# Performance work log

Measured on AMD Instinct MI355X. Metric: run time of the kernel, lower is better.

Reference implementation:

```python
import jax, jax.numpy as jnp
import numpy as np

B, N, D, DH = 2, 256, 256, 256


def setup_inputs() -> dict:
    key = jax.random.key(0)
    ks = jax.random.split(key, 8)
    s = 1.0 / np.sqrt(D)
    return {
        "x": jax.random.normal(ks[0], (B, N, D), dtype=jnp.float32),
        "e": jax.random.normal(ks[1], (B, N, N, D), dtype=jnp.float32),
        "Wq": jax.random.normal(ks[2], (D, DH), dtype=jnp.float32) * s,
        "bq": jnp.zeros((DH,), dtype=jnp.float32),
        "Wk": jax.random.normal(ks[3], (D, DH), dtype=jnp.float32) * s,
        "bk": jnp.zeros((DH,), dtype=jnp.float32),
        "Wv": jax.random.normal(ks[4], (D, DH), dtype=jnp.float32) * s,
        "bv": jnp.zeros((DH,), dtype=jnp.float32),
    }


def reference(x, e, Wq, bq, Wk, bk, Wv, bv):
    # Q_edge: [B, N, N, DH]; indexed Q[b, j, i, :]
    Q = jnp.einsum("bjid,dh->bjih", e, Wq) + bq
    K = x @ Wk + bk  # [B, N, DH]
    V = x @ Wv + bv  # [B, N, DH]
    scale = 1.0 / jnp.sqrt(jnp.asarray(Q.shape[-1], Q.dtype))
    # K_i[b,j,i] = K[b,i];  K_j[b,j,i] = K[b,j]  (torch expand semantics)
    att_i = jnp.exp(jnp.einsum("bjih,bih->bji", Q, K) * scale)
    att_j = jnp.exp(jnp.einsum("bjih,bjh->bji", Q, K) * scale)
    att_sum = att_i + att_j
    ai = att_i / att_sum  # dropout with p=0.0 is identity
    aj = att_j / att_sum
    # e_out[b,j,i] = ai*V[b,i] + aj*V[b,j]
    e_out = ai[..., None] * V[:, None, :, :] + aj[..., None] * V[:, :, None, :]
    return (x, e_out)
```

## Files before the change

### kernel.cpp

```cpp
#include <hip/hip_runtime.h>
#include <hip/hip_bf16.h>

typedef __bf16 bf16_t;
typedef bf16_t bf16x8 __attribute__((ext_vector_type(8)));
typedef float  f32x4  __attribute__((ext_vector_type(4)));

constexpr int Bc  = 2;
constexpr int Nc  = 256;
constexpr int Dc  = 256;
constexpr int DHc = 256;
constexpr int BM  = 64;
constexpr int NIB = Nc / BM;

__global__ void prep_kv(const float* __restrict__ x,
                        const float* __restrict__ Wk, const float* __restrict__ bk,
                        const float* __restrict__ Wv, const float* __restrict__ bv,
                        float* __restrict__ Kd, float* __restrict__ Vd) {
    constexpr int RPB = 4;
    __shared__ float xs[RPB][Dc];
    int r0 = blockIdx.x * RPB;
    int h  = threadIdx.x;
    for (int rr = 0; rr < RPB; ++rr)
        xs[rr][h] = x[(size_t)(r0 + rr) * Dc + h];
    __syncthreads();
    float bkv = bk[h], bvv = bv[h];
    float ka[RPB], va[RPB];
    #pragma unroll
    for (int rr = 0; rr < RPB; ++rr) { ka[rr] = bkv; va[rr] = bvv; }
    for (int d = 0; d < Dc; ++d) {
        float wk = Wk[(size_t)d * DHc + h];
        float wv = Wv[(size_t)d * DHc + h];
        #pragma unroll
        for (int rr = 0; rr < RPB; ++rr) {
            ka[rr] += xs[rr][d] * wk;
            va[rr] += xs[rr][d] * wv;
        }
    }
    #pragma unroll
    for (int rr = 0; rr < RPB; ++rr) {
        Kd[(size_t)(r0 + rr) * DHc + h] = ka[rr];
        Vd[(size_t)(r0 + rr) * DHc + h] = va[rr];
    }
}

__global__ void prep_wqt(const float* __restrict__ Wq, bf16_t* __restrict__ WqT) {
    int n = blockIdx.x;
    int d = threadIdx.x;
    WqT[(size_t)n * Dc + d] = (bf16_t)Wq[(size_t)d * DHc + n];
}

struct SMu {
    union {
        struct {
            bf16_t A[BM][Dc + 8];
            bf16_t Bt[DHc][40];
        } g;
        float Q[BM][DHc + 4];
    };
};

__global__ __launch_bounds__(256, 2)
void edge_attn(const float* __restrict__ e,
               const float* __restrict__ bq,
               const bf16_t* __restrict__ WqT,
               const float* __restrict__ Kd,
               const float* __restrict__ Vd,
               float* __restrict__ eout) {
    __shared__ SMu sm;
    __shared__ float s_kj[DHc], s_vj[DHc], s_bq[DHc];
    __shared__ float s_ri[BM][4], s_rj[BM][4];
    __shared__ float s_ai[BM], s_aj[BM];

    const int bid = blockIdx.x;
    const int b   = bid / (Nc * NIB);
    const int rem = bid % (Nc * NIB);
    const int j   = rem / NIB;
    const int i0  = (rem % NIB) * BM;
    const int tid = threadIdx.x;
    const int l   = tid & 63;
    const int w   = tid >> 6;
    const int lr  = l & 15;
    const int lk  = (l >> 4) * 8;

    {
        size_t off = ((size_t)b * Nc + j) * DHc + tid;
        s_kj[tid] = Kd[off];
        s_vj[tid] = Vd[off];
        s_bq[tid] = bq[tid];
    }

    const float4* e4 = reinterpret_cast<const float4*>(
        e + (((size_t)b * Nc + j) * Nc + i0) * Dc);
    #pragma unroll
    for (int q = 0; q < 16; ++q) {
        int f = tid + q * 256;
        float4 v = e4[f];
        int r = f >> 6;
        int c = (f & 63) * 4;
        union { bf16_t h[4]; uint2 u; } p;
        p.h[0] = (bf16_t)v.x; p.h[1] = (bf16_t)v.y;
        p.h[2] = (bf16_t)v.z; p.h[3] = (bf16_t)v.w;
        *reinterpret_cast<uint2*>(&sm.g.A[r][c]) = p.u;
    }

    f32x4 acc[4][4] = {};
    for (int ks = 0; ks < Dc / 32; ++ks) {
        const int k0 = ks * 32;
        __syncthreads();
        {
            const uint4* src = reinterpret_cast<const uint4*>(
                WqT + (size_t)tid * Dc + k0);
            uint4* dst = reinterpret_cast<uint4*>(&sm.g.Bt[tid][0]);
            dst[0] = src[0]; dst[1] = src[1]; dst[2] = src[2]; dst[3] = src[3];
        }
        __syncthreads();
        bf16x8 a[4], bb[4];
        #pragma unroll
        for (int m = 0; m < 4; ++m)
            a[m] = *reinterpret_cast<const bf16x8*>(&sm.g.A[m * 16 + lr][k0 + lk]);
        #pragma unroll
        for (int n = 0; n < 4; ++n)
            bb[n] = *reinterpret_cast<const bf16x8*>(&sm.g.Bt[w * 64 + n * 16 + lr][lk]);
        #pragma unroll
        for (int m = 0; m < 4; ++m)
            #pragma unroll
            for (int n = 0; n < 4; ++n)
                acc[m][n] = __builtin_amdgcn_mfma_f32_16x16x32_bf16(
                    a[m], bb[n], acc[m][n], 0, 0, 0);
    }
    __syncthreads();

    #pragma unroll
    for (int m = 0; m < 4; ++m) {
        int row0 = m * 16 + (l >> 4) * 4;
        #pragma unroll
        for (int n = 0; n < 4; ++n) {
            int col = w * 64 + n * 16 + lr;
            float bqv = s_bq[col];
            #pragma unroll
            for (int qq = 0; qq < 4; ++qq)
                sm.Q[row0 + qq][col] = acc[m][n][qq] + bqv;
        }
    }
    __syncthreads();

    {
        const int r = l;
        const int p = w;
        const float4* Krow = reinterpret_cast<const float4*>(
            Kd + (((size_t)b * Nc) + i0 + r) * DHc + p * 64);
        const float4* Qrow = reinterpret_cast<const float4*>(&sm.Q[r][p * 64]);
        const float4* Kj4  = reinterpret_cast<const float4*>(&s_kj[p * 64]);
        float si = 0.f, sj = 0.f;
        #pragma unroll
        for (int c4 = 0; c4 < 16; ++c4) {
            float4 qv = Qrow[c4];
            float4 ki = Krow[c4];
            float4 kj = Kj4[c4];
            si += qv.x * ki.x + qv.y * ki.y + qv.z * ki.z + qv.w * ki.w;
            sj += qv.x * kj.x + qv.y * kj.y + qv.z * kj.z + qv.w * kj.w;
        }
        s_ri[r][p] = si;
        s_rj[r][p] = sj;
    }
    __syncthreads();
    if (tid < BM) {
        float si = s_ri[tid][0] + s_ri[tid][1] + s_ri[tid][2] + s_ri[tid][3];
        float sj = s_rj[tid][0] + s_rj[tid][1] + s_rj[tid][2] + s_rj[tid][3];
        constexpr float scale = 0.0625f;
        float ai = 1.f / (1.f + __expf((sj - si) * scale));
        s_ai[tid] = ai;
        s_aj[tid] = 1.f - ai;
    }
    __syncthreads();

    {
        const int cg = (tid & 63) * 4;
        const int ro = tid >> 6;
        const float* Vb = Vd + ((size_t)b * Nc + i0) * DHc;
        float* ob = eout + (((size_t)b * Nc + j) * Nc + i0) * DHc;
        float4 vj = *reinterpret_cast<const float4*>(&s_vj[cg]);
        #pragma unroll
        for (int q = 0; q < 16; ++q) {
            int r = q * 4 + ro;
            float aiv = s_ai[r], ajv = s_aj[r];
            float4 vi = *reinterpret_cast<const float4*>(Vb + (size_t)r * DHc + cg);
            float4 o;
            o.x = aiv * vi.x + ajv * vj.x;
            o.y = aiv * vi.y + ajv * vj.y;
            o.z = aiv * vi.z + ajv * vj.z;
            o.w = aiv * vi.w + ajv * vj.w;
            *reinterpret_cast<float4*>(ob + (size_t)r * DHc + cg) = o;
        }
    }
}

extern "C" void kernel_launch(void* const* d_in, const int* in_sizes, int n_in,
                              void* d_out, int out_size, void* d_ws, size_t ws_size,
                              hipStream_t stream) {
    const float* x  = (const float*)d_in[0];
    const float* e  = (const float*)d_in[1];
    const float* Wq = (const float*)d_in[2];
    const float* bq = (const float*)d_in[3];
    const float* Wk = (const float*)d_in[4];
    const float* bk = (const float*)d_in[5];
    const float* Wv = (const float*)d_in[6];
    const float* bv = (const float*)d_in[7];
    float* out = (float*)d_out;

    float*  Kd  = (float*)d_ws;
    float*  Vd  = Kd + (size_t)Bc * Nc * DHc;
    bf16_t* WqT = (bf16_t*)(Vd + (size_t)Bc * Nc * DHc);

    hipMemcpyAsync(out, x, (size_t)Bc * Nc * Dc * sizeof(float),
                   hipMemcpyDeviceToDevice, stream);

    prep_kv<<<Bc * Nc / 4, 256, 0, stream>>>(x, Wk, bk, Wv, bv, Kd, Vd);
    prep_wqt<<<DHc, Dc, 0, stream>>>(Wq, WqT);
    edge_attn<<<Bc * Nc * NIB, 256, 0, stream>>>(
        e, bq, WqT, Kd, Vd, out + (size_t)Bc * Nc * Dc);
}
```

Measured before the change: 327.5 us.

## Fold Wq into K to replace edge GEMM with per-edge dot products

The score Q·K is rewritten as e·(Wq K) plus bq·K, so a prep kernel computes G = Wq·K (pre-scaled) and a bias term per node. The edge kernel then streams e once and takes two dot products per row with wavefront shuffle reductions, dropping the bf16 MFMA GEMM, the shared-memory staging and the Wq transpose kernel. The main kernel becomes a pure memory stream over e and the output, and it keeps full fp32 precision instead of bf16 for e.

```diff
diff --git a/kernel.cpp b/kernel.cpp
--- a/kernel.cpp
+++ b/kernel.cpp
@@ -1,9 +1,5 @@
 #include <hip/hip_runtime.h>
 #include <hip/hip_bf16.h>
-
-typedef __bf16 bf16_t;
-typedef bf16_t bf16x8 __attribute__((ext_vector_type(8)));
-typedef float  f32x4  __attribute__((ext_vector_type(4)));
 
 constexpr int Bc  = 2;
 constexpr int Nc  = 256;
@@ -12,65 +8,75 @@
 constexpr int BM  = 64;
 constexpr int NIB = Nc / BM;
 
-__global__ void prep_kv(const float* __restrict__ x,
-                        const float* __restrict__ Wk, const float* __restrict__ bk,
-                        const float* __restrict__ Wv, const float* __restrict__ bv,
-                        float* __restrict__ Kd, float* __restrict__ Vd) {
+__global__ __launch_bounds__(256)
+void prep_gvc(const float* __restrict__ x,
+              const float* __restrict__ Wq, const float* __restrict__ bq,
+              const float* __restrict__ Wk, const float* __restrict__ bk,
+              const float* __restrict__ Wv, const float* __restrict__ bv,
+              float* __restrict__ G, float* __restrict__ V, float* __restrict__ cc) {
     constexpr int RPB = 4;
+    constexpr float scale = 0.0625f;
     __shared__ float xs[RPB][Dc];
-    int r0 = blockIdx.x * RPB;
-    int h  = threadIdx.x;
+    __shared__ float ks[RPB][DHc];
+    const int r0 = blockIdx.x * RPB;
+    const int dd = threadIdx.x;
+
+    #pragma unroll
     for (int rr = 0; rr < RPB; ++rr)
-        xs[rr][h] = x[(size_t)(r0 + rr) * Dc + h];
+        xs[rr][dd] = x[(size_t)(r0 + rr) * Dc + dd];
     __syncthreads();
-    float bkv = bk[h], bvv = bv[h];
+
     float ka[RPB], va[RPB];
-    #pragma unroll
-    for (int rr = 0; rr < RPB; ++rr) { ka[rr] = bkv; va[rr] = bvv; }
-    for (int d = 0; d < Dc; ++d) {
-        float wk = Wk[(size_t)d * DHc + h];
-        float wv = Wv[(size_t)d * DHc + h];
+    {
+        float bkv = bk[dd], bvv = bv[dd];
+        #pragma unroll
+        for (int rr = 0; rr < RPB; ++rr) { ka[rr] = bkv; va[rr] = bvv; }
+    }
+    #pragma unroll 4
+    for (int d0 = 0; d0 < Dc; ++d0) {
+        float wk = Wk[(size_t)d0 * DHc + dd];
+        float wv = Wv[(size_t)d0 * DHc + dd];
         #pragma unroll
         for (int rr = 0; rr < RPB; ++rr) {
-            ka[rr] += xs[rr][d] * wk;
-            va[rr] += xs[rr][d] * wv;
+            ka[rr] += xs[rr][d0] * wk;
+            va[rr] += xs[rr][d0] * wv;
         }
     }
     #pragma unroll
     for (int rr = 0; rr < RPB; ++rr) {
-        Kd[(size_t)(r0 + rr) * DHc + h] = ka[rr];
-        Vd[(size_t)(r0 + rr) * DHc + h] = va[rr];
+        ks[rr][dd] = ka[rr];
+        V[(size_t)(r0 + rr) * DHc + dd] = va[rr];
+    }
+    __syncthreads();
+
+    float ga[RPB] = {};
+    #pragma unroll 8
+    for (int h = 0; h < DHc; ++h) {
+        float wq = Wq[(size_t)dd * DHc + h];
+        #pragma unroll
+        for (int rr = 0; rr < RPB; ++rr) ga[rr] += ks[rr][h] * wq;
+    }
+    #pragma unroll
+    for (int rr = 0; rr < RPB; ++rr)
+        G[(size_t)(r0 + rr) * Dc + dd] = ga[rr] * scale;
+
+    {
+        int rr = dd >> 6, l = dd & 63;
+        float p = 0.f;
+        #pragma unroll
+        for (int k = 0; k < 4; ++k) p += ks[rr][l + 64 * k] * bq[l + 64 * k];
+        #pragma unroll
+        for (int m = 1; m < 64; m <<= 1) p += __shfl_xor(p, m, 64);
+        if (l == 0) cc[r0 + rr] = p * scale;
     }
 }
 
-__global__ void prep_wqt(const float* __restrict__ Wq, bf16_t* __restrict__ WqT) {
-    int n = blockIdx.x;
-    int d = threadIdx.x;
-    WqT[(size_t)n * Dc + d] = (bf16_t)Wq[(size_t)d * DHc + n];
-}
-
-struct SMu {
-    union {
-        struct {
-            bf16_t A[BM][Dc + 8];
-            bf16_t Bt[DHc][40];
-        } g;
-        float Q[BM][DHc + 4];
-    };
-};
-
-__global__ __launch_bounds__(256, 2)
-void edge_attn(const float* __restrict__ e,
-               const float* __restrict__ bq,
-               const bf16_t* __restrict__ WqT,
-               const float* __restrict__ Kd,
-               const float* __restrict__ Vd,
+__global__ __launch_bounds__(256)
+void edge_main(const float* __restrict__ e,
+               const float* __restrict__ G,
+               const float* __restrict__ V,
+               const float* __restrict__ cc,
                float* __restrict__ eout) {
-    __shared__ SMu sm;
-    __shared__ float s_kj[DHc], s_vj[DHc], s_bq[DHc];
-    __shared__ float s_ri[BM][4], s_rj[BM][4];
-    __shared__ float s_ai[BM], s_aj[BM];
-
     const int bid = blockIdx.x;
     const int b   = bid / (Nc * NIB);
     const int rem = bid % (Nc * NIB);
@@ -79,119 +85,43 @@
     const int tid = threadIdx.x;
     const int l   = tid & 63;
     const int w   = tid >> 6;
-    const int lr  = l & 15;
-    const int lk  = (l >> 4) * 8;
 
-    {
-        size_t off = ((size_t)b * Nc + j) * DHc + tid;
-        s_kj[tid] = Kd[off];
-        s_vj[tid] = Vd[off];
-        s_bq[tid] = bq[tid];
-    }
+    const size_t nbase = (size_t)b * Nc;
+    const float4 gj = *reinterpret_cast<const float4*>(G + (nbase + j) * Dc + l * 4);
+    const float4 vj = *reinterpret_cast<const float4*>(V + (nbase + j) * DHc + l * 4);
+    const float  cj = cc[nbase + j];
 
-    const float4* e4 = reinterpret_cast<const float4*>(
-        e + (((size_t)b * Nc + j) * Nc + i0) * Dc);
-    #pragma unroll
-    for (int q = 0; q < 16; ++q) {
-        int f = tid + q * 256;
-        float4 v = e4[f];
-        int r = f >> 6;
-        int c = (f & 63) * 4;
-        union { bf16_t h[4]; uint2 u; } p;
-        p.h[0] = (bf16_t)v.x; p.h[1] = (bf16_t)v.y;
-        p.h[2] = (bf16_t)v.z; p.h[3] = (bf16_t)v.w;
-        *reinterpret_cast<uint2*>(&sm.g.A[r][c]) = p.u;
-    }
+    const int ibase = i0 + w * 16;
+    const float4* erow = reinterpret_cast<const float4*>(
+        e + (((size_t)b * Nc + j) * Nc + ibase) * Dc) + l;
+    const float4* Grow = reinterpret_cast<const float4*>(G + (nbase + ibase) * Dc) + l;
+    const float4* Vrow = reinterpret_cast<const float4*>(V + (nbase + ibase) * DHc) + l;
+    float4* orow = reinterpret_cast<float4*>(
+        eout + (((size_t)b * Nc + j) * Nc + ibase) * Dc) + l;
+    const float* ccp = cc + nbase + ibase;
 
-    f32x4 acc[4][4] = {};
-    for (int ks = 0; ks < Dc / 32; ++ks) {
-        const int k0 = ks * 32;
-        __syncthreads();
-        {
-            const uint4* src = reinterpret_cast<const uint4*>(
-                WqT + (size_t)tid * Dc + k0);
-            uint4* dst = reinterpret_cast<uint4*>(&sm.g.Bt[tid][0]);
-            dst[0] = src[0]; dst[1] = src[1]; dst[2] = src[2]; dst[3] = src[3];
+    #pragma unroll 4
+    for (int t = 0; t < 16; ++t) {
+        float4 ev = erow[(size_t)t * 64];
+        float4 gi = Grow[(size_t)t * 64];
+        float si = ev.x * gi.x + ev.y * gi.y + ev.z * gi.z + ev.w * gi.w;
+        float sj = ev.x * gj.x + ev.y * gj.y + ev.z * gj.z + ev.w * gj.w;
+        #pragma unroll
+        for (int m = 1; m < 64; m <<= 1) {
+            si += __shfl_xor(si, m, 64);
+            sj += __shfl_xor(sj, m, 64);
         }
-        __syncthreads();
-        bf16x8 a[4], bb[4];
-        #pragma unroll
-        for (int m = 0; m < 4; ++m)
-            a[m] = *reinterpret_cast<const bf16x8*>(&sm.g.A[m * 16 + lr][k0 + lk]);
-        #pragma unroll
-        for (int n = 0; n < 4; ++n)
-            bb[n] = *reinterpret_cast<const bf16x8*>(&sm.g.Bt[w * 64 + n * 16 + lr][lk]);
-        #pragma unroll
-        for (int m = 0; m < 4; ++m)
-            #pragma unroll
-            for (int n = 0; n < 4; ++n)
-                acc[m][n] = __builtin_amdgcn_mfma_f32_16x16x32_bf16(
-                    a[m], bb[n], acc[m][n], 0, 0, 0);
-    }
-    __syncthreads();
-
-    #pragma unroll
-    for (int m = 0; m < 4; ++m) {
-        int row0 = m * 16 + (l >> 4) * 4;
-        #pragma unroll
-        for (int n = 0; n < 4; ++n) {
-            int col = w * 64 + n * 16 + lr;
-            float bqv = s_bq[col];
-            #pragma unroll
-            for (int qq = 0; qq < 4; ++qq)
-                sm.Q[row0 + qq][col] = acc[m][n][qq] + bqv;
-        }
-    }
-    __syncthreads();
-
-    {
-        const int r = l;
-        const int p = w;
-        const float4* Krow = reinterpret_cast<const float4*>(
-            Kd + (((size_t)b * Nc) + i0 + r) * DHc + p * 64);
-        const float4* Qrow = reinterpret_cast<const float4*>(&sm.Q[r][p * 64]);
-        const float4* Kj4  = reinterpret_cast<const float4*>(&s_kj[p * 64]);
-        float si = 0.f, sj = 0.f;
-        #pragma unroll
-        for (int c4 = 0; c4 < 16; ++c4) {
-            float4 qv = Qrow[c4];
-            float4 ki = Krow[c4];
-            float4 kj = Kj4[c4];
-            si += qv.x * ki.x + qv.y * ki.y + qv.z * ki.z + qv.w * ki.w;
-            sj += qv.x * kj.x + qv.y * kj.y + qv.z * kj.z + qv.w * kj.w;
-        }
-        s_ri[r][p] = si;
-        s_rj[r][p] = sj;
-    }
-    __syncthreads();
-    if (tid < BM) {
-        float si = s_ri[tid][0] + s_ri[tid][1] + s_ri[tid][2] + s_ri[tid][3];
-        float sj = s_rj[tid][0] + s_rj[tid][1] + s_rj[tid][2] + s_rj[tid][3];
-        constexpr float scale = 0.0625f;
-        float ai = 1.f / (1.f + __expf((sj - si) * scale));
-        s_ai[tid] = ai;
-        s_aj[tid] = 1.f - ai;
-    }
-    __syncthreads();
-
-    {
-        const int cg = (tid & 63) * 4;
-        const int ro = tid >> 6;
-        const float* Vb = Vd + ((size_t)b * Nc + i0) * DHc;
-        float* ob = eout + (((size_t)b * Nc + j) * Nc + i0) * DHc;
-        float4 vj = *reinterpret_cast<const float4*>(&s_vj[cg]);
-        #pragma unroll
-        for (int q = 0; q < 16; ++q) {
-            int r = q * 4 + ro;
-            float aiv = s_ai[r], ajv = s_aj[r];
-            float4 vi = *reinterpret_cast<const float4*>(Vb + (size_t)r * DHc + cg);
-            float4 o;
-            o.x = aiv * vi.x + ajv * vj.x;
-            o.y = aiv * vi.y + ajv * vj.y;
-            o.z = aiv * vi.z + ajv * vj.z;
-            o.w = aiv * vi.w + ajv * vj.w;
-            *reinterpret_cast<float4*>(ob + (size_t)r * DHc + cg) = o;
-        }
+        si += ccp[t];
+        sj += cj;
+        float ai = 1.f / (1.f + __expf(sj - si));
+        float aj = 1.f - ai;
+        float4 vi = Vrow[(size_t)t * 64];
+        float4 o;
+        o.x = ai * vi.x + aj * vj.x;
+        o.y = ai * vi.y + aj * vj.y;
+        o.z = ai * vi.z + aj * vj.z;
+        o.w = ai * vi.w + aj * vj.w;
+        orow[(size_t)t * 64] = o;
     }
 }
 
@@ -208,15 +138,14 @@
     const float* bv = (const float*)d_in[7];
     float* out = (float*)d_out;
 
-    float*  Kd  = (float*)d_ws;
-    float*  Vd  = Kd + (size_t)Bc * Nc * DHc;
-    bf16_t* WqT = (bf16_t*)(Vd + (size_t)Bc * Nc * DHc);
+    float* G  = (float*)d_ws;
+    float* V  = G + (size_t)Bc * Nc * Dc;
+    float* cc = V + (size_t)Bc * Nc * DHc;
 
     hipMemcpyAsync(out, x, (size_t)Bc * Nc * Dc * sizeof(float),
                    hipMemcpyDeviceToDevice, stream);
 
-    prep_kv<<<Bc * Nc / 4, 256, 0, stream>>>(x, Wk, bk, Wv, bv, Kd, Vd);
-    prep_wqt<<<DHc, Dc, 0, stream>>>(Wq, WqT);
-    edge_attn<<<Bc * Nc * NIB, 256, 0, stream>>>(
-        e, bq, WqT, Kd, Vd, out + (size_t)Bc * Nc * Dc);
+    prep_gvc<<<Bc * Nc / 4, 256, 0, stream>>>(x, Wq, bq, Wk, bk, Wv, bv, G, V, cc);
+    edge_main<<<Bc * Nc * NIB, 256, 0, stream>>>(
+        e, G, V, cc, out + (size_t)Bc * Nc * Dc);
 }
```

New measurement: 306.6 us. 6.4% less time.
